# Performance work log

Measured on AMD Instinct MI355X. Metric: run time of the kernel, lower is better.

The kernel has to match this reference:

```python
import jax, jax.numpy as jnp
import numpy as np

N_HEAD = 16
N_KV_HEAD = 8
HEAD_DIM = 128
BLOCK_SIZE = 2048


def _rope_cache(T, hd):
    # faithful to torch: freqs repeat_interleave(2) along last dim
    inv_freq = 1.0 / (10000.0 ** (jnp.arange(0, hd, 2, dtype=jnp.float32) / hd))
    t = jnp.arange(T, dtype=jnp.float32)
    freqs = jnp.outer(t, inv_freq)            # [T, hd/2]
    freqs = jnp.repeat(freqs, 2, axis=-1)     # [T, hd]
    return jnp.cos(freqs), jnp.sin(freqs)


def _apply_rope(x, cos, sin):
    # x: [B, H, T, hd]; rotate-half convention from the torch code
    hd = x.shape[-1]
    x1, x2 = x[..., : hd // 2], x[..., hd // 2 :]
    x_rot = jnp.concatenate([-x2, x1], axis=-1)
    return x * cos + x_rot * sin


def setup_inputs() -> dict:
    key = jax.random.key(0)
    ks = jax.random.split(key, 5)
    B, T, C = 4, 2048, 2048
    kv_dim = N_KV_HEAD * HEAD_DIM
    s = 0.02
    return {
        "x": jax.random.normal(ks[0], (B, T, C), dtype=jnp.float32),
        "Wq": jax.random.normal(ks[1], (C, C), dtype=jnp.float32) * s,
        "Wk": jax.random.normal(ks[2], (kv_dim, C), dtype=jnp.float32) * s,
        "Wv": jax.random.normal(ks[3], (kv_dim, C), dtype=jnp.float32) * s,
        "Wo": jax.random.normal(ks[4], (C, C), dtype=jnp.float32) * s,
    }


def reference(x, Wq, Wk, Wv, Wo):
    B, T, C = x.shape
    hd = HEAD_DIM
    # projections (torch Linear: x @ W.T)
    q = (x @ Wq.T).reshape(B, T, N_HEAD, hd).transpose(0, 2, 1, 3)      # [B,H,T,hd]
    k = (x @ Wk.T).reshape(B, T, N_KV_HEAD, hd).transpose(0, 2, 1, 3)   # [B,Hkv,T,hd]
    v = (x @ Wv.T).reshape(B, T, N_KV_HEAD, hd).transpose(0, 2, 1, 3)

    cos, sin = _rope_cache(T, hd)  # start_pos = 0
    q = _apply_rope(q, cos, sin)
    k = _apply_rope(k, cos, sin)

    # GQA: repeat kv heads
    rep = N_HEAD // N_KV_HEAD
    k = jnp.repeat(k, rep, axis=1)  # [B,H,T,hd]
    v = jnp.repeat(v, rep, axis=1)

    scale = 1.0 / jnp.sqrt(jnp.float32(hd))
    scores = jnp.einsum("bhqd,bhkd->bhqk", q, k) * scale
    causal = jnp.tril(jnp.ones((T, T), dtype=bool))
    scores = jnp.where(causal, scores, jnp.finfo(scores.dtype).min)
    attn = jax.nn.softmax(scores, axis=-1)
    out = jnp.einsum("bhqk,bhkd->bhqd", attn, v)  # [B,H,T,hd]

    y = out.transpose(0, 2, 1, 3).reshape(B, T, C)
    return y @ Wo.T
```

## Files before the change

kernel.cpp:

```cpp
#include <hip/hip_runtime.h>

#define SCALE 0.08838834764831845f

typedef unsigned short bfu;
typedef __attribute__((ext_vector_type(8))) short bf16x8;
typedef __attribute__((ext_vector_type(4))) float f32x4;
typedef __attribute__((ext_vector_type(16))) float f32x16;

__device__ __forceinline__ unsigned short f2bf(float f) {
  unsigned int u = __float_as_uint(f);
  u += 0x7FFFu + ((u >> 16) & 1u);
  return (unsigned short)(u >> 16);
}
__device__ __forceinline__ float bf2f(unsigned short h) {
  return __uint_as_float(((unsigned int)h) << 16);
}
__device__ __forceinline__ unsigned int cvtpk(float a, float b) {
  unsigned int r;
  asm("v_cvt_pk_bf16_f32 %0, %1, %2" : "=v"(r) : "v"(a), "v"(b));
  return r;
}
__device__ __forceinline__ void pl32swap(unsigned int& a, unsigned int& b) {
  asm volatile("v_permlane32_swap_b32 %0, %1" : "+v"(a), "+v"(b));
}
__device__ __forceinline__ void async16(const void* g, void* l) {
  __builtin_amdgcn_global_load_lds(
      (const __attribute__((address_space(1))) unsigned int*)g,
      (__attribute__((address_space(3))) unsigned int*)l, 16, 0, 0);
}
__device__ __forceinline__ void barrier_sb() {
  __builtin_amdgcn_sched_barrier(0);
  __builtin_amdgcn_s_barrier();
  __builtin_amdgcn_sched_barrier(0);
}
__device__ __forceinline__ void wait0_bar() {
  __builtin_amdgcn_sched_barrier(0);
  asm volatile("s_waitcnt vmcnt(0)" ::: "memory");
  __builtin_amdgcn_s_barrier();
  __builtin_amdgcn_sched_barrier(0);
}

__global__ __launch_bounds__(256) void cvt_bf16(const float* __restrict__ src,
                                                bfu* __restrict__ dst, int n4) {
  int i = blockIdx.x * 256 + threadIdx.x;
  if (i >= n4) return;
  float4 v = ((const float4*)src)[i];
  ushort4 o;
  o.x = f2bf(v.x); o.y = f2bf(v.y); o.z = f2bf(v.z); o.w = f2bf(v.w);
  ((ushort4*)dst)[i] = o;
}

__global__ __launch_bounds__(256) void rope_table(float2* __restrict__ tab) {
  int idx = blockIdx.x * 256 + threadIdx.x;
  int t = idx >> 6, f = idx & 63;
  const float nl = -0.14391156463f;
  float th = (float)t * expf((float)f * nl);
  tab[idx] = make_float2(cosf(th), sinf(th));
}

__device__ __forceinline__ void storeC(float* p, float v) { *p = v; }
__device__ __forceinline__ void storeC(bfu* p, float v) { *p = f2bf(v); }

template <typename OutT, bool FUSE>
__global__ __launch_bounds__(512, 2) void gemm256(
    const bfu* __restrict__ A, const bfu* __restrict__ B,
    OutT* __restrict__ C, const float2* __restrict__ ropeTab,
    bfu* __restrict__ qTo, bfu* __restrict__ kTo, bfu* __restrict__ vTo,
    int M, int N, int K) {
  __shared__ __align__(16) char smem[131072];
  const int tid = threadIdx.x;
  const int w = tid >> 6, l = tid & 63;
  const int lr = l & 15, lg = l >> 4;
  const int wr = w >> 2, wc = w & 3;

  const int nm = gridDim.x, nn = gridDim.y;
  const int flat = blockIdx.y * nm + blockIdx.x;
  const int xcd = flat & 7, j = flat >> 3;
  const int RM = (nm * nn) >> 5;
  const int nregm = nm / RM;
  const int m0 = ((xcd % nregm) * RM + (j >> 2)) * 256;
  const int n0 = ((xcd / nregm) * 4 + (j & 3)) * 256;

  const int sr = l >> 3;
  const int sc = (l & 7) ^ sr;
  auto stageHalf = [&](const bfu* G, int grow0, int kcol, char* lds) {
#pragma unroll
    for (int jj = 0; jj < 2; jj++) {
      int row = (jj * 8 + w) * 8 + sr;
      async16(G + (size_t)(grow0 + row) * K + kcol + sc * 8,
              lds + (jj * 8 + w) * 1024 + l * 16);
    }
  };

  f32x4 acc[8][4];
#pragma unroll
  for (int i = 0; i < 8; i++)
#pragma unroll
    for (int jj = 0; jj < 4; jj++) acc[i][jj] = (f32x4){0.f, 0.f, 0.f, 0.f};

  stageHalf(A, m0, 0, smem);
  stageHalf(A, m0 + 128, 0, smem + 16384);
  stageHalf(B, n0, 0, smem + 65536);
  stageHalf(B, n0 + 128, 0, smem + 65536 + 16384);

  const int KT = K >> 6;
  const int swiz = (lr & 7) << 4;
  const int cbase = (wc >> 1) * 128 + (wc & 1) * 32;
#pragma unroll 1
  for (int t = 0; t < KT; t++) {
    const int bt = t & 1;
    const char* Ah = smem + bt * 32768 + wr * 16384;
    const char* Bt = smem + 65536 + bt * 32768;
    char* An = smem + (bt ^ 1) * 32768;
    char* Bn = smem + 65536 + (bt ^ 1) * 32768;
    const bool pfch = (t + 1 < KT);
    const int kn = (t + 1) << 6;

    if (pfch) {
      stageHalf(A, m0, kn, An);
      asm volatile("s_waitcnt vmcnt(2)" ::: "memory");
    } else {
      asm volatile("s_waitcnt vmcnt(0)" ::: "memory");
    }
    barrier_sb();

    bf16x8 bfr[4][2];
#pragma unroll
    for (int n = 0; n < 4; n++) {
      const char* rowp =
          Bt + (cbase + (n & 1) * 16 + (n >> 1) * 64 + lr) * 128;
#pragma unroll
      for (int s = 0; s < 2; s++)
        bfr[n][s] = *(const bf16x8*)(rowp + ((((s << 2) + lg) << 4) ^ swiz));
    }

#pragma unroll
    for (int p = 0; p < 4; p++) {
      bf16x8 af[2][2];
#pragma unroll
      for (int m2 = 0; m2 < 2; m2++) {
        const char* rowp = Ah + ((p * 2 + m2) * 16 + lr) * 128;
#pragma unroll
        for (int s = 0; s < 2; s++)
          af[m2][s] = *(const bf16x8*)(rowp + ((((s << 2) + lg) << 4) ^ swiz));
      }
      if (pfch) {
        if (p == 1) stageHalf(A, m0 + 128, kn, An + 16384);
        if (p == 2) stageHalf(B, n0, kn, Bn);
        if (p == 3) stageHalf(B, n0 + 128, kn, Bn + 16384);
      }
      __builtin_amdgcn_s_setprio(1);
#pragma unroll
      for (int m2 = 0; m2 < 2; m2++)
#pragma unroll
        for (int n = 0; n < 4; n++)
#pragma unroll
          for (int s = 0; s < 2; s++)
            acc[p * 2 + m2][n] = __builtin_amdgcn_mfma_f32_16x16x32_bf16(
                af[m2][s], bfr[n][s], acc[p * 2 + m2][n], 0, 0, 0);
      __builtin_amdgcn_s_setprio(0);
    }
    barrier_sb();
  }

  if constexpr (!FUSE) {
#pragma unroll
    for (int i = 0; i < 8; i++)
#pragma unroll
      for (int jj = 0; jj < 4; jj++)
#pragma unroll
        for (int r = 0; r < 4; r++) {
          int gm = m0 + wr * 128 + i * 16 + lg * 4 + r;
          int gn = n0 + cbase + (jj & 1) * 16 + (jj >> 1) * 64 + lr;
          storeC(&C[(size_t)gm * N + gn], acc[i][jj][r]);
        }
  } else {
    const int head = (n0 >> 7) + (wc >> 1);
    if (head < 24) {
#pragma unroll
      for (int i = 0; i < 8; i++)
#pragma unroll
        for (int r = 0; r < 4; r++) {
          int gm = m0 + wr * 128 + i * 16 + lg * 4 + r;
          int tt = gm & 2047, bb = gm >> 11;
          bfu* rowp = (head < 16)
                          ? qTo + (((size_t)((bb * 16 + head) * 2048 + tt)) << 7)
                          : kTo + (((size_t)((bb * 8 + head - 16) * 2048 + tt)) << 7);
          const float2* trow = ropeTab + tt * 64;
#pragma unroll
          for (int n = 0; n < 2; n++) {
            int d = (wc & 1) * 32 + n * 16 + lr;
            int i1 = d >> 1;
            float2 cs1 = trow[i1];
            float2 cs2 = trow[i1 + 32];
            float x1 = acc[i][n][r], x2 = acc[i][n + 2][r];
            rowp[d] = f2bf(x1 * cs1.x - x2 * cs1.y);
            rowp[d + 64] = f2bf(x2 * cs2.x + x1 * cs2.y);
          }
        }
    } else {
      const int kh = head - 24;
#pragma unroll
      for (int i = 0; i < 8; i++) {
        int gm0 = m0 + wr * 128 + i * 16 + lg * 4;
        int t0 = gm0 & 2047, bb = gm0 >> 11;
#pragma unroll
        for (int n = 0; n < 4; n++) {
          int d = (wc & 1) * 32 + (n & 1) * 16 + (n >> 1) * 64 + lr;
          bfu* p = vTo + (((size_t)((bb * 8 + kh) * 128 + d)) << 11) + t0;
          ushort4 o;
          o.x = f2bf(acc[i][n][0]);
          o.y = f2bf(acc[i][n][1]);
          o.z = f2bf(acc[i][n][2]);
          o.w = f2bf(acc[i][n][3]);
          *(ushort4*)p = o;
        }
      }
    }
  }
}

__global__ __launch_bounds__(512, 2) void gemm128(const bfu* __restrict__ A,
                                                  const bfu* __restrict__ B,
                                                  float* __restrict__ C,
                                                  int M, int N, int K) {
  __shared__ __align__(16) char smem[65536];
  const int tid = threadIdx.x;
  const int w = tid >> 6, l = tid & 63;
  const int lr = l & 15, lg = l >> 4;
  const int wr = w >> 2, wc = w & 3;

  const int nm = gridDim.x, nn = gridDim.y;
  const int flat = blockIdx.y * nm + blockIdx.x;
  const int xcd = flat & 7, j = flat >> 3;
  const int RM = (nm * nn) >> 5;
  const int nregm = nm / RM;
  const int m0 = ((xcd % nregm) * RM + (j >> 2)) * 128;
  const int n0 = ((xcd / nregm) * 4 + (j & 3)) * 128;

  const int sr = l >> 3;
  const int sc = (l & 7) ^ sr;
  auto stageHalf = [&](const bfu* G, int grow0, int kcol, char* lds) {
#pragma unroll
    for (int jj = 0; jj < 2; jj++) {
      int row = (jj * 8 + w) * 8 + sr;
      async16(G + (size_t)(grow0 + row) * K + kcol + sc * 8,
              lds + (jj * 8 + w) * 1024 + l * 16);
    }
  };

  f32x4 acc[4][2];
#pragma unroll
  for (int i = 0; i < 4; i++)
#pragma unroll
    for (int n = 0; n < 2; n++) acc[i][n] = (f32x4){0.f, 0.f, 0.f, 0.f};

  stageHalf(A, m0, 0, smem);
  stageHalf(B, n0, 0, smem + 32768);

  const int KT = K >> 6;
  const int swiz = (lr & 7) << 4;
#pragma unroll 1
  for (int t = 0; t < KT; t++) {
    const int bt = t & 1;
    const char* Ah = smem + bt * 16384;
    const char* Bt = smem + 32768 + bt * 16384;
    char* An = smem + (bt ^ 1) * 16384;
    char* Bn = smem + 32768 + (bt ^ 1) * 16384;
    const bool pfch = (t + 1 < KT);
    const int kn = (t + 1) << 6;

    if (pfch) {
      stageHalf(A, m0, kn, An);
      asm volatile("s_waitcnt vmcnt(2)" ::: "memory");
    } else {
      asm volatile("s_waitcnt vmcnt(0)" ::: "memory");
    }
    barrier_sb();

    bf16x8 bfr[2][2];
#pragma unroll
    for (int n = 0; n < 2; n++) {
      const char* rowp = Bt + (wc * 32 + n * 16 + lr) * 128;
#pragma unroll
      for (int s = 0; s < 2; s++)
        bfr[n][s] = *(const bf16x8*)(rowp + ((((s << 2) + lg) << 4) ^ swiz));
    }

#pragma unroll
    for (int p = 0; p < 4; p++) {
      bf16x8 af[2];
      const char* rowp = Ah + (wr * 64 + p * 16 + lr) * 128;
#pragma unroll
      for (int s = 0; s < 2; s++)
        af[s] = *(const bf16x8*)(rowp + ((((s << 2) + lg) << 4) ^ swiz));
      if (p == 2 && pfch) stageHalf(B, n0, kn, Bn);
      __builtin_amdgcn_s_setprio(1);
#pragma unroll
      for (int n = 0; n < 2; n++)
#pragma unroll
        for (int s = 0; s < 2; s++)
          acc[p][n] = __builtin_amdgcn_mfma_f32_16x16x32_bf16(
              af[s], bfr[n][s], acc[p][n], 0, 0, 0);
      __builtin_amdgcn_s_setprio(0);
    }
    barrier_sb();
  }

#pragma unroll
  for (int i = 0; i < 4; i++)
#pragma unroll
    for (int n = 0; n < 2; n++)
#pragma unroll
      for (int r = 0; r < 4; r++) {
        int gm = m0 + wr * 64 + i * 16 + lg * 4 + r;
        int gn = n0 + wc * 32 + n * 16 + lr;
        C[(size_t)gm * N + gn] = acc[i][n][r];
      }
}

__global__ __launch_bounds__(512, 2) void flash_attn7(const bfu* __restrict__ qT,
                                                      const bfu* __restrict__ kT,
                                                      const bfu* __restrict__ vT,
                                                      bfu* __restrict__ attn) {
  __shared__ __align__(16) char smem[65536];
  const int tid = threadIdx.x;
  const int w = tid >> 6, l = tid & 63;
  const int ln = l & 31, h2 = l >> 5;
  const int hsw = w >> 2, w4 = w & 3;
  const int idx = blockIdx.x;
  const int khb = idx & 31;
  const int pg = idx >> 5;
  const int kh = khb & 7, b = khb >> 3;
  const int hh = kh * 2 + hsw;
  const int nkbA = 2 * pg + 2;
  const int NT = 34;

  const bfu* Qh = qT + ((size_t)(b * 16 + hh) * 2048) * 128;
  const bfu* Kb = kT + ((size_t)(b * 8 + kh) * 2048) * 128;
  const bfu* Vb = vT + ((size_t)(b * 8 + kh) * 128) * 2048;

  auto stageK = [&](int buf, int t) {
    char* Kl = smem + buf * 16384;
    const bfu* src = Kb + (size_t)t * 64 * 128;
#pragma unroll
    for (int ii = 0; ii < 2; ii++) {
      int i = w * 2 + ii;
      int row = i * 4 + (l >> 4);
      int ck = (l & 15) ^ (row & 15);
      async16(src + row * 128 + ck * 8, Kl + i * 1024 + l * 16);
    }
  };
  auto stageV = [&](int buf, int t) {
    char* Vl = smem + 32768 + buf * 16384;
    const bfu* src = Vb + t * 64;
#pragma unroll
    for (int jj = 0; jj < 2; jj++) {
      int j = w * 2 + jj;
      int row = j * 8 + (l >> 3);
      int ck = (l & 7) ^ (row & 7);
      async16(src + (size_t)row * 2048 + ck * 8, Vl + j * 1024 + l * 16);
    }
  };

  int qrow0 = pg * 128 + w4 * 32;

  bf16x8 qf[8];
#pragma unroll
  for (int dt = 0; dt < 8; dt++)
    qf[dt] = *(const bf16x8*)(Qh + (size_t)(qrow0 + ln) * 128 + dt * 16 + h2 * 8);

  f32x16 O[4];
#pragma unroll
  for (int mt = 0; mt < 4; mt++)
#pragma unroll
    for (int r = 0; r < 16; r++) O[mt][r] = 0.f;
  float li = 0.f;

  auto flush = [&]() {
    float ls = li + __shfl_xor(li, 32);
    float inv = 1.f / ls;
    bfu* orow = attn + ((size_t)(b * 2048 + qrow0 + ln)) * 2048 + hh * 128;
#pragma unroll
    for (int mt = 0; mt < 4; mt++)
#pragma unroll
      for (int g = 0; g < 4; g++) {
        unsigned int r0 = cvtpk(O[mt][g * 4 + 0] * inv, O[mt][g * 4 + 1] * inv);
        unsigned int r1 = cvtpk(O[mt][g * 4 + 2] * inv, O[mt][g * 4 + 3] * inv);
        uint2 o; o.x = r0; o.y = r1;
        *(uint2*)(orow + mt * 32 + g * 8 + h2 * 4) = o;
      }
  };

  stageK(0, 0);
  stageV(0, 0);

#pragma unroll 1
  for (int t = 0; t < NT; t++) {
    wait0_bar();
    if (t + 1 < NT) {
      const int kn = (t + 1 >= nkbA) ? (t + 1 - nkbA) : (t + 1);
      stageK((t + 1) & 1, kn);
      stageV((t + 1) & 1, kn);
    }

    if (t == nkbA) {
      flush();
      qrow0 = (15 - pg) * 128 + w4 * 32;
#pragma unroll
      for (int dt = 0; dt < 8; dt++)
        qf[dt] =
            *(const bf16x8*)(Qh + (size_t)(qrow0 + ln) * 128 + dt * 16 + h2 * 8);
#pragma unroll
      for (int mt = 0; mt < 4; mt++)
#pragma unroll
        for (int r = 0; r < 16; r++) O[mt][r] = 0.f;
      li = 0.f;
    }

    const int k0 = ((t >= nkbA) ? (t - nkbA) : t) * 64;
    const int myrow = qrow0 + ln;
    if (k0 <= qrow0 + 31) {
      const char* Kl = smem + (t & 1) * 16384;
      const char* Vl = smem + 32768 + (t & 1) * 16384;

      f32x16 S0, S1;
#pragma unroll
      for (int r = 0; r < 16; r++) { S0[r] = 0.f; S1[r] = 0.f; }
      const int swk = (ln & 15) << 4;
      __builtin_amdgcn_s_setprio(1);
#pragma unroll
      for (int dt = 0; dt < 8; dt++) {
        bf16x8 kf0 =
            *(const bf16x8*)(Kl + ln * 256 + ((dt * 32 + h2 * 16) ^ swk));
        bf16x8 kf1 = *(const bf16x8*)(Kl + (32 + ln) * 256 +
                                      ((dt * 32 + h2 * 16) ^ swk));
        S0 = __builtin_amdgcn_mfma_f32_32x32x16_bf16(kf0, qf[dt], S0, 0, 0, 0);
        S1 = __builtin_amdgcn_mfma_f32_32x32x16_bf16(kf1, qf[dt], S1, 0, 0, 0);
      }
      __builtin_amdgcn_s_setprio(0);

      const bool need_mask = (k0 + 63) > qrow0;
      bf16x8 pfr[4];
#pragma unroll
      for (int half = 0; half < 2; half++) {
        float p[16];
#pragma unroll
        for (int r = 0; r < 16; r++) {
          float s = half ? S1[r] : S0[r];
          float pv = __builtin_exp2f(fmaf(s, 0.12751743f, -17.312340f));
          if (need_mask) {
            int key = k0 + half * 32 + (r & 3) + 8 * (r >> 2) + 4 * h2;
            if (key > myrow) pv = 0.f;
          }
          p[r] = pv;
          li += pv;
        }
#pragma unroll
        for (int kt = 0; kt < 2; kt++) {
          const float* q = p + kt * 8;
          unsigned int a0 = cvtpk(q[0], q[1]);
          unsigned int a1 = cvtpk(q[2], q[3]);
          unsigned int b0 = cvtpk(q[4], q[5]);
          unsigned int b1 = cvtpk(q[6], q[7]);
          pl32swap(a0, b0);
          pl32swap(a1, b1);
          union { unsigned int u[4]; bf16x8 v; } c;
          c.u[0] = a0; c.u[1] = a1; c.u[2] = b0; c.u[3] = b1;
          pfr[half * 2 + kt] = c.v;
        }
      }

      const int swv = (ln & 7) << 4;
      __builtin_amdgcn_s_setprio(1);
#pragma unroll
      for (int mt = 0; mt < 4; mt++) {
        const char* vb = Vl + (mt * 32 + ln) * 128;
#pragma unroll
        for (int kt = 0; kt < 4; kt++) {
          bf16x8 vf = *(const bf16x8*)(vb + ((kt * 32 + h2 * 16) ^ swv));
          O[mt] = __builtin_amdgcn_mfma_f32_32x32x16_bf16(vf, pfr[kt], O[mt], 0, 0, 0);
        }
      }
      __builtin_amdgcn_s_setprio(0);
    }
  }

  flush();
}

extern "C" void kernel_launch(void* const* d_in, const int* in_sizes, int n_in,
                              void* d_out, int out_size, void* d_ws, size_t ws_size,
                              hipStream_t stream) {
  const float* x = (const float*)d_in[0];
  const float* Wq = (const float*)d_in[1];
  const float* Wk = (const float*)d_in[2];
  const float* Wv = (const float*)d_in[3];
  const float* Wo = (const float*)d_in[4];
  float* out = (float*)d_out;
  char* ws = (char*)d_ws;

  bfu* xb     = (bfu*)(ws);
  bfu* Wqkv   = (bfu*)(ws + 33554432);
  bfu* Wob    = (bfu*)(ws + 50331648);
  float2* tab = (float2*)(ws + 58720256);
  bfu* qT     = (bfu*)(ws + 125829120);
  bfu* kT     = (bfu*)(ws + 159383552);
  bfu* vT     = (bfu*)(ws + 176160768);
  bfu* attn = xb;

  cvt_bf16<<<16384, 256, 0, stream>>>(x, xb, 4194304);
  cvt_bf16<<<4096, 256, 0, stream>>>(Wq, Wqkv, 1048576);
  cvt_bf16<<<2048, 256, 0, stream>>>(Wk, Wqkv + (size_t)2048 * 2048, 524288);
  cvt_bf16<<<2048, 256, 0, stream>>>(Wv, Wqkv + (size_t)3072 * 2048, 524288);
  cvt_bf16<<<4096, 256, 0, stream>>>(Wo, Wob, 1048576);
  rope_table<<<512, 256, 0, stream>>>(tab);

  gemm256<bfu, true><<<dim3(32, 16), 512, 0, stream>>>(
      xb, Wqkv, (bfu*)nullptr, tab, qT, kT, vT, 8192, 4096, 2048);
  flash_attn7<<<256, 512, 0, stream>>>(qT, kT, vT, attn);
  gemm128<<<dim3(64, 16), 512, 0, stream>>>(attn, Wob, out, 8192, 2048, 2048);
}
```

Baseline: 468.3 us.

## Split paired causal query tiles into separate blocks and fuse weight conversions

The attention kernel previously paired a short and a long causal query tile in one block (34 iterations each) for load balance. Now each of 512 blocks handles a single 128-row query tile, iterating only over its causal key range, with heavy tiles scheduled first. This doubles grid parallelism and removes the mid-loop flush and Q reload, but relies on the hardware scheduler for balance. The four weight conversion launches are also merged into one kernel to cut launch overhead.

```diff
diff --git a/kernel.cpp b/kernel.cpp
--- a/kernel.cpp
+++ b/kernel.cpp
@@ -48,6 +48,22 @@
   ushort4 o;
   o.x = f2bf(v.x); o.y = f2bf(v.y); o.z = f2bf(v.z); o.w = f2bf(v.w);
   ((ushort4*)dst)[i] = o;
+}
+
+__global__ __launch_bounds__(256) void cvt_weights(
+    const float* __restrict__ Wq, const float* __restrict__ Wk,
+    const float* __restrict__ Wv, const float* __restrict__ Wo,
+    bfu* __restrict__ Wqkv, bfu* __restrict__ Wob) {
+  int i = blockIdx.x * 256 + threadIdx.x;
+  const float* src; bfu* dst; int off;
+  if (i < 1048576)      { src = Wq; dst = Wqkv;            off = i; }
+  else if (i < 1572864) { src = Wk; dst = Wqkv + 4194304;  off = i - 1048576; }
+  else if (i < 2097152) { src = Wv; dst = Wqkv + 6291456;  off = i - 1572864; }
+  else                  { src = Wo; dst = Wob;             off = i - 2097152; }
+  float4 v = ((const float4*)src)[off];
+  ushort4 o;
+  o.x = f2bf(v.x); o.y = f2bf(v.y); o.z = f2bf(v.z); o.w = f2bf(v.w);
+  ((ushort4*)dst)[off] = o;
 }
 
 __global__ __launch_bounds__(256) void rope_table(float2* __restrict__ tab) {
@@ -319,7 +335,7 @@
       }
 }
 
-__global__ __launch_bounds__(512, 2) void flash_attn7(const bfu* __restrict__ qT,
+__global__ __launch_bounds__(512, 2) void flash_attn8(const bfu* __restrict__ qT,
                                                       const bfu* __restrict__ kT,
                                                       const bfu* __restrict__ vT,
                                                       bfu* __restrict__ attn) {
@@ -330,11 +346,12 @@
   const int hsw = w >> 2, w4 = w & 3;
   const int idx = blockIdx.x;
   const int khb = idx & 31;
-  const int pg = idx >> 5;
+  const int qt = 15 - (idx >> 5);
   const int kh = khb & 7, b = khb >> 3;
   const int hh = kh * 2 + hsw;
-  const int nkbA = 2 * pg + 2;
-  const int NT = 34;
+  const int NT = 2 * qt + 2;
+  const int qrow0 = qt * 128 + w4 * 32;
+  const int myrow = qrow0 + ln;
 
   const bfu* Qh = qT + ((size_t)(b * 16 + hh) * 2048) * 128;
   const bfu* Kb = kT + ((size_t)(b * 8 + kh) * 2048) * 128;
@@ -363,12 +380,10 @@
     }
   };
 
-  int qrow0 = pg * 128 + w4 * 32;
-
   bf16x8 qf[8];
 #pragma unroll
   for (int dt = 0; dt < 8; dt++)
-    qf[dt] = *(const bf16x8*)(Qh + (size_t)(qrow0 + ln) * 128 + dt * 16 + h2 * 8);
+    qf[dt] = *(const bf16x8*)(Qh + (size_t)myrow * 128 + dt * 16 + h2 * 8);
 
   f32x16 O[4];
 #pragma unroll
@@ -376,21 +391,6 @@
 #pragma unroll
     for (int r = 0; r < 16; r++) O[mt][r] = 0.f;
   float li = 0.f;
-
-  auto flush = [&]() {
-    float ls = li + __shfl_xor(li, 32);
-    float inv = 1.f / ls;
-    bfu* orow = attn + ((size_t)(b * 2048 + qrow0 + ln)) * 2048 + hh * 128;
-#pragma unroll
-    for (int mt = 0; mt < 4; mt++)
-#pragma unroll
-      for (int g = 0; g < 4; g++) {
-        unsigned int r0 = cvtpk(O[mt][g * 4 + 0] * inv, O[mt][g * 4 + 1] * inv);
-        unsigned int r1 = cvtpk(O[mt][g * 4 + 2] * inv, O[mt][g * 4 + 3] * inv);
-        uint2 o; o.x = r0; o.y = r1;
-        *(uint2*)(orow + mt * 32 + g * 8 + h2 * 4) = o;
-      }
-  };
 
   stageK(0, 0);
   stageV(0, 0);
@@ -399,27 +399,11 @@
   for (int t = 0; t < NT; t++) {
     wait0_bar();
     if (t + 1 < NT) {
-      const int kn = (t + 1 >= nkbA) ? (t + 1 - nkbA) : (t + 1);
-      stageK((t + 1) & 1, kn);
-      stageV((t + 1) & 1, kn);
-    }
-
-    if (t == nkbA) {
-      flush();
-      qrow0 = (15 - pg) * 128 + w4 * 32;
-#pragma unroll
-      for (int dt = 0; dt < 8; dt++)
-        qf[dt] =
-            *(const bf16x8*)(Qh + (size_t)(qrow0 + ln) * 128 + dt * 16 + h2 * 8);
-#pragma unroll
-      for (int mt = 0; mt < 4; mt++)
-#pragma unroll
-        for (int r = 0; r < 16; r++) O[mt][r] = 0.f;
-      li = 0.f;
-    }
-
-    const int k0 = ((t >= nkbA) ? (t - nkbA) : t) * 64;
-    const int myrow = qrow0 + ln;
+      stageK((t + 1) & 1, t + 1);
+      stageV((t + 1) & 1, t + 1);
+    }
+
+    const int k0 = t * 64;
     if (k0 <= qrow0 + 31) {
       const char* Kl = smem + (t & 1) * 16384;
       const char* Vl = smem + 32768 + (t & 1) * 16384;
@@ -486,7 +470,18 @@
     }
   }
 
-  flush();
+  li += __shfl_xor(li, 32);
+  const float inv = 1.f / li;
+  bfu* orow = attn + ((size_t)(b * 2048 + qrow0 + ln)) * 2048 + hh * 128;
+#pragma unroll
+  for (int mt = 0; mt < 4; mt++)
+#pragma unroll
+    for (int g = 0; g < 4; g++) {
+      unsigned int r0 = cvtpk(O[mt][g * 4 + 0] * inv, O[mt][g * 4 + 1] * inv);
+      unsigned int r1 = cvtpk(O[mt][g * 4 + 2] * inv, O[mt][g * 4 + 3] * inv);
+      uint2 o; o.x = r0; o.y = r1;
+      *(uint2*)(orow + mt * 32 + g * 8 + h2 * 4) = o;
+    }
 }
 
 extern "C" void kernel_launch(void* const* d_in, const int* in_sizes, int n_in,
@@ -510,14 +505,11 @@
   bfu* attn = xb;
 
   cvt_bf16<<<16384, 256, 0, stream>>>(x, xb, 4194304);
-  cvt_bf16<<<4096, 256, 0, stream>>>(Wq, Wqkv, 1048576);
-  cvt_bf16<<<2048, 256, 0, stream>>>(Wk, Wqkv + (size_t)2048 * 2048, 524288);
-  cvt_bf16<<<2048, 256, 0, stream>>>(Wv, Wqkv + (size_t)3072 * 2048, 524288);
-  cvt_bf16<<<4096, 256, 0, stream>>>(Wo, Wob, 1048576);
+  cvt_weights<<<12288, 256, 0, stream>>>(Wq, Wk, Wv, Wo, Wqkv, Wob);
   rope_table<<<512, 256, 0, stream>>>(tab);
 
   gemm256<bfu, true><<<dim3(32, 16), 512, 0, stream>>>(
       xb, Wqkv, (bfu*)nullptr, tab, qT, kT, vT, 8192, 4096, 2048);
-  flash_attn7<<<256, 512, 0, stream>>>(qT, kT, vT, attn);
+  flash_attn8<<<512, 512, 0, stream>>>(qT, kT, vT, attn);
   gemm128<<<dim3(64, 16), 512, 0, stream>>>(attn, Wob, out, 8192, 2048, 2048);
 }
```

New measurement: 450.8 us. 3.7% less time.
